# Kernel tuning notes

Measured on AMD Instinct MI355X. Metric: run time of the kernel, lower is better.

The kernel has to match this reference:

```python
import jax, jax.numpy as jnp
import numpy as np

B, N, E = 2, 50000, 800000
IN, HID, OUT = 128, 64, 1
EPS = 1e-5


def setup_inputs() -> dict:
    key = jax.random.key(0)
    ks = jax.random.split(key, 13)
    x = jax.random.normal(ks[0], (B, N, IN), jnp.float32)
    edge_index = jax.random.randint(ks[1], (2, E), 0, N, dtype=jnp.int64)
    edge_weight = 0.1 * jax.random.normal(ks[2], (E,), jnp.float32)  # nn.Parameter, pre-exp
    W1 = jax.random.normal(ks[3], (IN, HID), jnp.float32) / np.sqrt(IN)
    b1 = jnp.zeros((HID,), jnp.float32)
    W2 = jax.random.normal(ks[4], (HID, HID), jnp.float32) / np.sqrt(HID)
    b2 = jnp.zeros((HID,), jnp.float32)
    g1 = jnp.ones((HID,), jnp.float32)
    be1 = jnp.zeros((HID,), jnp.float32)
    g2 = jnp.ones((HID,), jnp.float32)
    be2 = jnp.zeros((HID,), jnp.float32)
    Wc = jax.random.normal(ks[5], (HID, OUT), jnp.float32) / np.sqrt(HID)
    bc = jnp.zeros((OUT,), jnp.float32)
    return {"x": x, "edge_weight": edge_weight, "W1": W1, "b1": b1,
            "W2": W2, "b2": b2, "g1": g1, "be1": be1, "g2": g2, "be2": be2,
            "Wc": Wc, "bc": bc, "edge_index": edge_index}


def reference(x, edge_weight, W1, b1, W2, b2, g1, be1, g2, be2, Wc, bc, edge_index):
    n = x.shape[1]
    row, col = edge_index[0], edge_index[1]
    ew = jnp.exp(edge_weight)
    # GCN normalization with self-loops (fill_value=1), as in PyG gcn_norm
    loop = jnp.arange(n)
    rows = jnp.concatenate([row, loop])
    cols = jnp.concatenate([col, loop])
    w = jnp.concatenate([ew, jnp.ones((n,), ew.dtype)])
    deg = jax.ops.segment_sum(w, cols, num_segments=n)
    dinv = 1.0 / jnp.sqrt(deg)  # deg >= 1 due to self-loops
    norm = dinv[rows] * w * dinv[cols]  # [E+N]

    def conv(h, W, b):
        h = h @ W                                  # [B, N, H]
        msg = h[:, rows, :] * norm[None, :, None]  # gather + weight  [B, E+N, H]
        agg = jnp.zeros_like(h).at[:, cols, :].add(msg)  # scatter-add
        return agg + b

    def bn(h, g, be):  # BatchNorm1d over flattened (B*N, H), training-mode stats
        h2 = h.reshape(-1, h.shape[-1])
        m = h2.mean(axis=0)
        v = h2.var(axis=0)
        return (((h2 - m) / jnp.sqrt(v + EPS)) * g + be).reshape(h.shape)

    h = jax.nn.relu(conv(x, W1, b1))
    h = bn(h, g1, be1)  # dropout is identity in eval
    h = jax.nn.relu(conv(h, W2, b2))
    h = bn(h, g2, be2)
    out = (h @ Wc + bc)[..., 0]  # squeeze(-1) -> [B, N]
    return out
```

## Files before the change

kernel.cpp:

```cpp
#include <hip/hip_runtime.h>
#include <hip/hip_fp16.h>
#include <cstdint>
#include <cstddef>


#define CAP  64
#define OCAP 65536
#define BN_EPS 1e-5f

static __device__ __forceinline__ unsigned h2u(__half2 h) {
  union { __half2 h; unsigned u; } c; c.h = h; return c.u;
}
static __device__ __forceinline__ __half2 u2h(unsigned u) {
  union { unsigned u; __half2 h; } c; c.u = u; return c.h;
}

__global__ void k_fill(const float* __restrict__ ew, const int* __restrict__ ei,
                       int* __restrict__ cnt, int2* __restrict__ pairs,
                       int* __restrict__ ofl_cnt, int* __restrict__ ofl_list, int E) {
  int i0 = blockIdx.x * 1024 + threadIdx.x;
  int r[4], c[4];
  float w[4];
  bool ok[4];
#pragma unroll
  for (int j = 0; j < 4; ++j) {
    int e = i0 + j * 256;
    ok[j] = e < E;
    if (ok[j]) {
      r[j] = ei[e];
      c[j] = ei[(size_t)E + e];
      w[j] = expf(ew[e]);
    }
  }
  int pos[4];
#pragma unroll
  for (int j = 0; j < 4; ++j)
    if (ok[j]) pos[j] = atomicAdd(&cnt[c[j]], 1);
#pragma unroll
  for (int j = 0; j < 4; ++j) {
    if (!ok[j]) continue;
    if (pos[j] < CAP) {
      pairs[(size_t)c[j] * CAP + pos[j]] = make_int2(r[j], __float_as_int(w[j]));
    } else {
      int o = atomicAdd(ofl_cnt, 1);
      if (o < OCAP) ofl_list[o] = i0 + j * 256;
    }
  }
}

__global__ void k_degb(const int2* __restrict__ pairs, const int* __restrict__ cnt,
                       float* __restrict__ deg, int N) {
  int node = blockIdx.x * 4 + (threadIdx.x >> 6);
  if (node >= N) return;
  int lane = threadIdx.x & 63;
  int n = cnt[node];
  n = n > CAP ? CAP : n;
  float v = 0.0f;
  if (lane < n) v = __int_as_float(pairs[(size_t)node * CAP + lane].y);
#pragma unroll
  for (int off = 32; off > 0; off >>= 1) v += __shfl_xor(v, off, 64);
  if (lane == 0) deg[node] = v + 1.0f;
}

__global__ void k_dego(const float* __restrict__ ew, const int* __restrict__ ei,
                       const int* __restrict__ ofl_cnt, const int* __restrict__ ofl_list,
                       float* __restrict__ deg, int E) {
  int tot = *ofl_cnt;
  if (tot > OCAP) tot = OCAP;
  for (int i = blockIdx.x * blockDim.x + threadIdx.x; i < tot;
       i += gridDim.x * blockDim.x) {
    int e = ofl_list[i];
    atomicAdd(&deg[ei[(size_t)E + e]], expf(ew[e]));
  }
}

__global__ void k_dinvf(float* __restrict__ deg, int N) {
  int i = blockIdx.x * blockDim.x + threadIdx.x;
  if (i < N) deg[i] = rsqrtf(deg[i]);
}

template<int CIN, bool TR, bool PERM>
__global__ void k_gemm(const void* __restrict__ in_, const float* __restrict__ W,
                       __half* __restrict__ out, int nrows, int N,
                       const float* __restrict__ bias, const float* __restrict__ scsh) {
  constexpr int RT = 64;
  constexpr int KC = 64;
  constexpr int NCH = CIN / KC;
  constexpr int S = KC + 4;
  __shared__ float ws[KC * 64];
  __shared__ float xs[RT * S];

  int tid = threadIdx.x;
  int row0 = blockIdx.x * RT;
  int rg = tid >> 4;
  int cg = tid & 15;
  int c0 = cg * 4;
  int r0 = rg * 4;

  float acc[4][4];
#pragma unroll
  for (int i = 0; i < 4; ++i)
#pragma unroll
    for (int j = 0; j < 4; ++j) acc[i][j] = 0.0f;

  for (int ch = 0; ch < NCH; ++ch) {
    if (ch) __syncthreads();
    const float4* Wp = (const float4*)(W + (size_t)ch * KC * 64);
    for (int s = tid; s < KC * 16; s += 256)
      ((float4*)ws)[s] = Wp[s];
    for (int s = tid; s < RT * 16; s += 256) {
      int r = s >> 4, k4 = s & 15;
      int gr = row0 + r;
      int kg = ch * KC + k4 * 4;
      float4 v = make_float4(0.f, 0.f, 0.f, 0.f);
      if (gr < nrows) {
        if (TR) {
          const __half* in = (const __half*)in_;
          uint2 u = *(const uint2*)(in + (size_t)gr * CIN + kg);
          float2 fa = __half22float2(u2h(u.x));
          float2 fb = __half22float2(u2h(u.y));
          v = make_float4(fa.x, fa.y, fb.x, fb.y);
        } else {
          const float* in = (const float*)in_;
          v = *(const float4*)(in + (size_t)gr * CIN + kg);
        }
      }
      if (TR) {
        float4 bb = *(const float4*)(bias + kg);
        float4 sc = *(const float4*)(scsh + kg);
        float4 sh = *(const float4*)(scsh + 64 + kg);
        v.x = fmaxf(v.x + bb.x, 0.f) * sc.x + sh.x;
        v.y = fmaxf(v.y + bb.y, 0.f) * sc.y + sh.y;
        v.z = fmaxf(v.z + bb.z, 0.f) * sc.z + sh.z;
        v.w = fmaxf(v.w + bb.w, 0.f) * sc.w + sh.w;
      }
      *(float4*)&xs[r * S + k4 * 4] = v;
    }
    __syncthreads();

#pragma unroll 2
    for (int kk = 0; kk < KC; kk += 4) {
      float4 wv0 = *(const float4*)&ws[(kk + 0) * 64 + c0];
      float4 wv1 = *(const float4*)&ws[(kk + 1) * 64 + c0];
      float4 wv2 = *(const float4*)&ws[(kk + 2) * 64 + c0];
      float4 wv3 = *(const float4*)&ws[(kk + 3) * 64 + c0];
#pragma unroll
      for (int i = 0; i < 4; ++i) {
        float4 xv = *(const float4*)&xs[(r0 + i) * S + kk];
        acc[i][0] = fmaf(xv.x, wv0.x, acc[i][0]);
        acc[i][1] = fmaf(xv.x, wv0.y, acc[i][1]);
        acc[i][2] = fmaf(xv.x, wv0.z, acc[i][2]);
        acc[i][3] = fmaf(xv.x, wv0.w, acc[i][3]);
        acc[i][0] = fmaf(xv.y, wv1.x, acc[i][0]);
        acc[i][1] = fmaf(xv.y, wv1.y, acc[i][1]);
        acc[i][2] = fmaf(xv.y, wv1.z, acc[i][2]);
        acc[i][3] = fmaf(xv.y, wv1.w, acc[i][3]);
        acc[i][0] = fmaf(xv.z, wv2.x, acc[i][0]);
        acc[i][1] = fmaf(xv.z, wv2.y, acc[i][1]);
        acc[i][2] = fmaf(xv.z, wv2.z, acc[i][2]);
        acc[i][3] = fmaf(xv.z, wv2.w, acc[i][3]);
        acc[i][0] = fmaf(xv.w, wv3.x, acc[i][0]);
        acc[i][1] = fmaf(xv.w, wv3.y, acc[i][1]);
        acc[i][2] = fmaf(xv.w, wv3.z, acc[i][2]);
        acc[i][3] = fmaf(xv.w, wv3.w, acc[i][3]);
      }
    }
  }

#pragma unroll
  for (int i = 0; i < 4; ++i) {
    int gr = row0 + r0 + i;
    if (gr < nrows) {
      int orow = PERM ? ((gr < N) ? gr * 2 : (gr - N) * 2 + 1) : gr;
      __half2 h01 = __floats2half2_rn(acc[i][0], acc[i][1]);
      __half2 h23 = __floats2half2_rn(acc[i][2], acc[i][3]);
      *(uint2*)(out + (size_t)orow * 64 + c0) = make_uint2(h2u(h01), h2u(h23));
    }
  }
}

__global__ void k_agg(const __half* __restrict__ h, const int2* __restrict__ pairs,
                      const int* __restrict__ cnt, const float* __restrict__ dinv,
                      __half* __restrict__ raw, int N) {
  int node = blockIdx.x * 4 + (threadIdx.x >> 6);
  if (node >= N) return;
  int lane = threadIdx.x & 63;
  const __half2* hv = (const __half2*)h;
  float dc = dinv[node];
  float2 self = __half22float2(hv[(size_t)node * 64 + lane]);
  float2 acc = make_float2(self.x * dc, self.y * dc);
  int n = cnt[node];
  n = n > CAP ? CAP : n;
  const int2* pp = pairs + (size_t)node * CAP;
  int k = 0;
  for (; k + 8 <= n; k += 8) {
    int2 p[8];
#pragma unroll
    for (int q = 0; q < 8; ++q) p[q] = pp[k + q];
    float dr[8];
#pragma unroll
    for (int q = 0; q < 8; ++q) dr[q] = dinv[p[q].x];
    __half2 v[8];
#pragma unroll
    for (int q = 0; q < 8; ++q) v[q] = hv[(size_t)p[q].x * 64 + lane];
#pragma unroll
    for (int q = 0; q < 8; ++q) {
      float w = __int_as_float(p[q].y) * dr[q];
      float2 f = __half22float2(v[q]);
      acc.x = fmaf(w, f.x, acc.x);
      acc.y = fmaf(w, f.y, acc.y);
    }
  }
  for (; k < n; ++k) {
    int2 p = pp[k];
    float w = __int_as_float(p.y) * dinv[p.x];
    float2 f = __half22float2(hv[(size_t)p.x * 64 + lane]);
    acc.x = fmaf(w, f.x, acc.x);
    acc.y = fmaf(w, f.y, acc.y);
  }
  ((__half2*)raw)[(size_t)node * 64 + lane] =
      __floats2half2_rn(acc.x * dc, acc.y * dc);
}

__global__ void k_ofl(const float* __restrict__ ew, const int* __restrict__ ei,
                      const float* __restrict__ dinv, const int* __restrict__ ofl_cnt,
                      const int* __restrict__ ofl_list,
                      const __half* __restrict__ h, __half* __restrict__ raw,
                      int N, int E) {
  int tot = *ofl_cnt;
  if (tot > OCAP) tot = OCAP;
  for (int i = blockIdx.x * blockDim.x + threadIdx.x; i < tot;
       i += gridDim.x * blockDim.x) {
    int e = ofl_list[i];
    int r = ei[e];
    int c = ei[(size_t)E + e];
    float nrm = dinv[r] * expf(ew[e]) * dinv[c];
    const __half2* hr = (const __half2*)(h + (size_t)r * 128);
    unsigned* dst = (unsigned*)(raw + (size_t)c * 128);
    for (int j = 0; j < 64; ++j) {
      float2 hv2 = __half22float2(hr[j]);
      unsigned old = dst[j], assumed;
      do {
        assumed = old;
        float2 cur = __half22float2(u2h(assumed));
        __half2 nv = __floats2half2_rn(cur.x + nrm * hv2.x, cur.y + nrm * hv2.y);
        old = atomicCAS(&dst[j], assumed, h2u(nv));
      } while (old != assumed);
    }
  }
}

__global__ void k_stats(const __half* __restrict__ raw, const float* __restrict__ bias,
                        float* __restrict__ stats, int rows) {
  __shared__ float S[256], Q[256];
  int tid = threadIdx.x;
  int c = tid & 63, rg = tid >> 6;
  float s = 0.0f, q = 0.0f;
  for (int r = blockIdx.x * 4 + rg; r < rows; r += gridDim.x * 4) {
    float y = fmaxf(__half2float(raw[(size_t)r * 64 + c]) + bias[c], 0.0f);
    s += y;
    q += y * y;
  }
  S[tid] = s; Q[tid] = q;
  __syncthreads();
  if (tid < 64) {
    float ts = S[tid] + S[tid + 64] + S[tid + 128] + S[tid + 192];
    float tq = Q[tid] + Q[tid + 64] + Q[tid + 128] + Q[tid + 192];
    atomicAdd(&stats[tid], ts);
    atomicAdd(&stats[64 + tid], tq);
  }
}

__global__ void k_scale(const float* __restrict__ stats, const float* __restrict__ g,
                        const float* __restrict__ be, float* __restrict__ scsh,
                        float invCnt) {
  int c = threadIdx.x;
  if (c >= 64) return;
  float m = stats[c] * invCnt;
  float v = stats[64 + c] * invCnt - m * m;
  v = v < 0.0f ? 0.0f : v;
  float inv = rsqrtf(v + BN_EPS);
  float sc = g[c] * inv;
  scsh[c] = sc;
  scsh[64 + c] = be[c] - m * sc;
}

__global__ void k_out(const __half* __restrict__ raw, const float* __restrict__ bias,
                      const float* __restrict__ scsh, const float* __restrict__ Wc,
                      const float* __restrict__ bc, float* __restrict__ out,
                      int rows, int N) {
  int row = blockIdx.x * 4 + (threadIdx.x >> 6);
  int c = threadIdx.x & 63;
  if (row >= rows) return;
  float v = fmaxf(__half2float(raw[(size_t)row * 64 + c]) + bias[c], 0.0f)
              * scsh[c] + scsh[64 + c];
  float p = v * Wc[c];
#pragma unroll
  for (int off = 32; off > 0; off >>= 1) p += __shfl_xor(p, off, 64);
  if (c == 0) {
    int node = row >> 1, b = row & 1;
    out[(size_t)b * N + node] = p + bc[0];
  }
}

extern "C" void kernel_launch(void* const* d_in, const int* in_sizes, int n_in,
                              void* d_out, int out_size, void* d_ws, size_t ws_size,
                              hipStream_t stream) {
  const float* x   = (const float*)d_in[0];
  const float* ew  = (const float*)d_in[1];
  const float* W1  = (const float*)d_in[2];
  const float* b1  = (const float*)d_in[3];
  const float* W2  = (const float*)d_in[4];
  const float* b2  = (const float*)d_in[5];
  const float* g1  = (const float*)d_in[6];
  const float* be1 = (const float*)d_in[7];
  const float* g2  = (const float*)d_in[8];
  const float* be2 = (const float*)d_in[9];
  const float* Wc  = (const float*)d_in[10];
  const float* bc  = (const float*)d_in[11];
  const int*   ei  = (const int*)d_in[12];

  const int E  = in_sizes[1];
  const int BN = in_sizes[0] / 128;
  const int N  = BN / 2;

  char* w = (char*)d_ws;
  size_t off = 0;
  float* dinv   = (float*)(w + off); off += (size_t)N * 4;
  int*   cnt    = (int*)  (w + off); off += (size_t)N * 4;
  float* stats1 = (float*)(w + off); off += 512;
  float* stats2 = (float*)(w + off); off += 512;
  int*   oflc   = (int*)  (w + off); off += 16;
  size_t zbytes = off;
  float* scsh1  = (float*)(w + off); off += 512;
  float* scsh2  = (float*)(w + off); off += 512;
  int*   ofll   = (int*)  (w + off); off += (size_t)OCAP * 4;
  off = (off + 255) & ~(size_t)255;
  int2*   pairs = (int2*)  (w + off); off += (size_t)N * CAP * 8;
  __half* bufA  = (__half*)(w + off); off += (size_t)BN * 64 * 2;
  __half* bufB  = (__half*)(w + off); off += (size_t)BN * 64 * 2;

  float* out = (float*)d_out;

  hipMemsetAsync(w, 0, zbytes, stream);

  dim3 blk(256);
  int gE4 = (E + 1023) / 1024;
  int gN  = (N + 255) / 256;
  int gG  = (BN + 63) / 64;
  int gR  = (BN + 3) / 4;
  int gA  = (N + 3) / 4;

  k_fill<<<gE4, blk, 0, stream>>>(ew, ei, cnt, pairs, oflc, ofll, E);
  k_degb<<<gA, blk, 0, stream>>>(pairs, cnt, dinv, N);
  k_dego<<<16, blk, 0, stream>>>(ew, ei, oflc, ofll, dinv, E);
  k_dinvf<<<gN, blk, 0, stream>>>(dinv, N);

  k_gemm<128, false, true><<<gG, blk, 0, stream>>>(x, W1, bufA, BN, N, nullptr, nullptr);
  k_agg<<<gA, blk, 0, stream>>>(bufA, pairs, cnt, dinv, bufB, N);
  k_ofl<<<16, blk, 0, stream>>>(ew, ei, dinv, oflc, ofll, bufA, bufB, N, E);
  k_stats<<<400, blk, 0, stream>>>(bufB, b1, stats1, BN);
  k_scale<<<1, 64, 0, stream>>>(stats1, g1, be1, scsh1, 1.0f / (float)BN);

  k_gemm<64, true, false><<<gG, blk, 0, stream>>>(bufB, W2, bufA, BN, N, b1, scsh1);
  k_agg<<<gA, blk, 0, stream>>>(bufA, pairs, cnt, dinv, bufB, N);
  k_ofl<<<16, blk, 0, stream>>>(ew, ei, dinv, oflc, ofll, bufA, bufB, N, E);
  k_stats<<<400, blk, 0, stream>>>(bufB, b2, stats2, BN);
  k_scale<<<1, 64, 0, stream>>>(stats2, g2, be2, scsh2, 1.0f / (float)BN);

  k_out<<<gR, blk, 0, stream>>>(bufB, b2, scsh2, Wc, bc, out, BN, N);
}
```

Baseline: 362.4 us.

## Fuse first GEMM with edge fill, pack edge pairs to 32 bits, fold BN scale

Combines the first-layer GEMM and the edge bucketing fill into one launch, with blocks interleaved by role so the compute-bound and atomic-bound work can overlap. Edge pairs are packed into a single 32-bit word: a 16-bit source index and an fp16 weight. This halves the pair storage and gather traffic in the degree and aggregation kernels, but assumes node ids fit in 16 bits and rounds weights to half precision. The BN scale/shift computation moves into the last block of the stats kernel via a completion counter, removing two launches. The aggregation unroll is also widened to 12 with a 4-wide tail.

After: 366.5 us. Within noise of the previous version (+1.1%).

```diff
diff --git a/kernel.cpp b/kernel.cpp
--- a/kernel.cpp
+++ b/kernel.cpp
@@ -14,41 +14,113 @@
 static __device__ __forceinline__ __half2 u2h(unsigned u) {
   union { unsigned u; __half2 h; } c; c.u = u; return c.h;
 }
-
-__global__ void k_fill(const float* __restrict__ ew, const int* __restrict__ ei,
-                       int* __restrict__ cnt, int2* __restrict__ pairs,
-                       int* __restrict__ ofl_cnt, int* __restrict__ ofl_list, int E) {
-  int i0 = blockIdx.x * 1024 + threadIdx.x;
-  int r[4], c[4];
-  float w[4];
-  bool ok[4];
-#pragma unroll
-  for (int j = 0; j < 4; ++j) {
-    int e = i0 + j * 256;
-    ok[j] = e < E;
-    if (ok[j]) {
-      r[j] = ei[e];
-      c[j] = ei[(size_t)E + e];
-      w[j] = expf(ew[e]);
-    }
-  }
-  int pos[4];
-#pragma unroll
-  for (int j = 0; j < 4; ++j)
-    if (ok[j]) pos[j] = atomicAdd(&cnt[c[j]], 1);
-#pragma unroll
-  for (int j = 0; j < 4; ++j) {
-    if (!ok[j]) continue;
-    if (pos[j] < CAP) {
-      pairs[(size_t)c[j] * CAP + pos[j]] = make_int2(r[j], __float_as_int(w[j]));
+static __device__ __forceinline__ unsigned pack_pair(int src, float w) {
+  __half hw = __float2half_rn(w);
+  union { __half h; unsigned short s; } c; c.h = hw;
+  return ((unsigned)src << 16) | c.s;
+}
+static __device__ __forceinline__ float pair_w(unsigned p) {
+  union { unsigned short s; __half h; } c; c.s = (unsigned short)(p & 0xFFFFu);
+  return __half2float(c.h);
+}
+
+__global__ void k_mega(const float* __restrict__ x, const float* __restrict__ W,
+                       __half* __restrict__ out, int nrows, int N,
+                       const float* __restrict__ ew, const int* __restrict__ ei,
+                       int* __restrict__ cnt, unsigned* __restrict__ pairs,
+                       int* __restrict__ ofl_cnt, int* __restrict__ ofl_list,
+                       int E, int gemmBlocks, int fillBlocks) {
+  constexpr int RT = 64, KC = 64, S = KC + 4;
+  __shared__ float ws[KC * 64];
+  __shared__ float xs[RT * S];
+
+  int bid = blockIdx.x;
+  int tid = threadIdx.x;
+  int role = bid % 3;
+
+  if (role == 0) {
+    int gid = bid / 3;
+    if (gid >= gemmBlocks) return;
+    int row0 = gid * RT;
+    int rg = tid >> 4, cg = tid & 15;
+    int c0 = cg * 4, r0 = rg * 4;
+    float acc[4][4];
+#pragma unroll
+    for (int i = 0; i < 4; ++i)
+#pragma unroll
+      for (int j = 0; j < 4; ++j) acc[i][j] = 0.0f;
+
+    for (int ch = 0; ch < 2; ++ch) {
+      if (ch) __syncthreads();
+      const float4* Wp = (const float4*)(W + (size_t)ch * KC * 64);
+      for (int s = tid; s < KC * 16; s += 256)
+        ((float4*)ws)[s] = Wp[s];
+      for (int s = tid; s < RT * 16; s += 256) {
+        int r = s >> 4, k4 = s & 15;
+        int gr = row0 + r;
+        float4 v = make_float4(0.f, 0.f, 0.f, 0.f);
+        if (gr < nrows)
+          v = *(const float4*)(x + (size_t)gr * 128 + ch * KC + k4 * 4);
+        *(float4*)&xs[r * S + k4 * 4] = v;
+      }
+      __syncthreads();
+#pragma unroll 2
+      for (int kk = 0; kk < KC; kk += 4) {
+        float4 wv0 = *(const float4*)&ws[(kk + 0) * 64 + c0];
+        float4 wv1 = *(const float4*)&ws[(kk + 1) * 64 + c0];
+        float4 wv2 = *(const float4*)&ws[(kk + 2) * 64 + c0];
+        float4 wv3 = *(const float4*)&ws[(kk + 3) * 64 + c0];
+#pragma unroll
+        for (int i = 0; i < 4; ++i) {
+          float4 xv = *(const float4*)&xs[(r0 + i) * S + kk];
+          acc[i][0] = fmaf(xv.x, wv0.x, acc[i][0]);
+          acc[i][1] = fmaf(xv.x, wv0.y, acc[i][1]);
+          acc[i][2] = fmaf(xv.x, wv0.z, acc[i][2]);
+          acc[i][3] = fmaf(xv.x, wv0.w, acc[i][3]);
+          acc[i][0] = fmaf(xv.y, wv1.x, acc[i][0]);
+          acc[i][1] = fmaf(xv.y, wv1.y, acc[i][1]);
+          acc[i][2] = fmaf(xv.y, wv1.z, acc[i][2]);
+          acc[i][3] = fmaf(xv.y, wv1.w, acc[i][3]);
+          acc[i][0] = fmaf(xv.z, wv2.x, acc[i][0]);
+          acc[i][1] = fmaf(xv.z, wv2.y, acc[i][1]);
+          acc[i][2] = fmaf(xv.z, wv2.z, acc[i][2]);
+          acc[i][3] = fmaf(xv.z, wv2.w, acc[i][3]);
+          acc[i][0] = fmaf(xv.w, wv3.x, acc[i][0]);
+          acc[i][1] = fmaf(xv.w, wv3.y, acc[i][1]);
+          acc[i][2] = fmaf(xv.w, wv3.z, acc[i][2]);
+          acc[i][3] = fmaf(xv.w, wv3.w, acc[i][3]);
+        }
+      }
+    }
+#pragma unroll
+    for (int i = 0; i < 4; ++i) {
+      int gr = row0 + r0 + i;
+      if (gr < nrows) {
+        int orow = (gr < N) ? gr * 2 : (gr - N) * 2 + 1;
+        __half2 h01 = __floats2half2_rn(acc[i][0], acc[i][1]);
+        __half2 h23 = __floats2half2_rn(acc[i][2], acc[i][3]);
+        *(uint2*)(out + (size_t)orow * 64 + c0) = make_uint2(h2u(h01), h2u(h23));
+      }
+    }
+  } else {
+    int fid = (bid / 3) * 2 + role - 1;
+    if (fid >= fillBlocks) return;
+    int e = fid * 256 + tid;
+    if (e >= E) return;
+    int r = ei[e];
+    int c = ei[(size_t)E + e];
+    float w = expf(ew[e]);
+    int pos = atomicAdd(&cnt[c], 1);
+    if (pos < CAP) {
+      pairs[(size_t)c * CAP + pos] = pack_pair(r, w);
     } else {
       int o = atomicAdd(ofl_cnt, 1);
-      if (o < OCAP) ofl_list[o] = i0 + j * 256;
-    }
-  }
-}
-
-__global__ void k_degb(const int2* __restrict__ pairs, const int* __restrict__ cnt,
+      if (o < OCAP) ofl_list[o] = e;
+    }
+  }
+}
+
+__global__ void k_degb(const unsigned* __restrict__ pairs, const int* __restrict__ cnt,
                        float* __restrict__ deg, int N) {
   int node = blockIdx.x * 4 + (threadIdx.x >> 6);
   if (node >= N) return;
@@ -56,7 +128,7 @@
   int n = cnt[node];
   n = n > CAP ? CAP : n;
   float v = 0.0f;
-  if (lane < n) v = __int_as_float(pairs[(size_t)node * CAP + lane].y);
+  if (lane < n) v = pair_w(pairs[(size_t)node * CAP + lane]);
 #pragma unroll
   for (int off = 32; off > 0; off >>= 1) v += __shfl_xor(v, off, 64);
   if (lane == 0) deg[node] = v + 1.0f;
@@ -79,107 +151,85 @@
   if (i < N) deg[i] = rsqrtf(deg[i]);
 }
 
-template<int CIN, bool TR, bool PERM>
-__global__ void k_gemm(const void* __restrict__ in_, const float* __restrict__ W,
-                       __half* __restrict__ out, int nrows, int N,
-                       const float* __restrict__ bias, const float* __restrict__ scsh) {
-  constexpr int RT = 64;
-  constexpr int KC = 64;
-  constexpr int NCH = CIN / KC;
-  constexpr int S = KC + 4;
+__global__ void k_gemm2(const __half* __restrict__ in, const float* __restrict__ W,
+                        __half* __restrict__ out, int nrows,
+                        const float* __restrict__ bias, const float* __restrict__ scsh) {
+  constexpr int RT = 64, KC = 64, S = KC + 4;
   __shared__ float ws[KC * 64];
   __shared__ float xs[RT * S];
 
   int tid = threadIdx.x;
   int row0 = blockIdx.x * RT;
-  int rg = tid >> 4;
-  int cg = tid & 15;
-  int c0 = cg * 4;
-  int r0 = rg * 4;
-
+  for (int s = tid; s < KC * 16; s += 256)
+    ((float4*)ws)[s] = ((const float4*)W)[s];
+  for (int s = tid; s < RT * 16; s += 256) {
+    int r = s >> 4, k4 = s & 15;
+    int gr = row0 + r;
+    int kg = k4 * 4;
+    float4 v = make_float4(0.f, 0.f, 0.f, 0.f);
+    if (gr < nrows) {
+      uint2 u = *(const uint2*)(in + (size_t)gr * 64 + kg);
+      float2 fa = __half22float2(u2h(u.x));
+      float2 fb = __half22float2(u2h(u.y));
+      v = make_float4(fa.x, fa.y, fb.x, fb.y);
+    }
+    float4 bb = *(const float4*)(bias + kg);
+    float4 sc = *(const float4*)(scsh + kg);
+    float4 sh = *(const float4*)(scsh + 64 + kg);
+    v.x = fmaxf(v.x + bb.x, 0.f) * sc.x + sh.x;
+    v.y = fmaxf(v.y + bb.y, 0.f) * sc.y + sh.y;
+    v.z = fmaxf(v.z + bb.z, 0.f) * sc.z + sh.z;
+    v.w = fmaxf(v.w + bb.w, 0.f) * sc.w + sh.w;
+    *(float4*)&xs[r * S + kg] = v;
+  }
+  __syncthreads();
+
+  int rg = tid >> 4, cg = tid & 15;
+  int c0 = cg * 4, r0 = rg * 4;
   float acc[4][4];
 #pragma unroll
   for (int i = 0; i < 4; ++i)
 #pragma unroll
     for (int j = 0; j < 4; ++j) acc[i][j] = 0.0f;
-
-  for (int ch = 0; ch < NCH; ++ch) {
-    if (ch) __syncthreads();
-    const float4* Wp = (const float4*)(W + (size_t)ch * KC * 64);
-    for (int s = tid; s < KC * 16; s += 256)
-      ((float4*)ws)[s] = Wp[s];
-    for (int s = tid; s < RT * 16; s += 256) {
-      int r = s >> 4, k4 = s & 15;
-      int gr = row0 + r;
-      int kg = ch * KC + k4 * 4;
-      float4 v = make_float4(0.f, 0.f, 0.f, 0.f);
-      if (gr < nrows) {
-        if (TR) {
-          const __half* in = (const __half*)in_;
-          uint2 u = *(const uint2*)(in + (size_t)gr * CIN + kg);
-          float2 fa = __half22float2(u2h(u.x));
-          float2 fb = __half22float2(u2h(u.y));
-          v = make_float4(fa.x, fa.y, fb.x, fb.y);
-        } else {
-          const float* in = (const float*)in_;
-          v = *(const float4*)(in + (size_t)gr * CIN + kg);
-        }
-      }
-      if (TR) {
-        float4 bb = *(const float4*)(bias + kg);
-        float4 sc = *(const float4*)(scsh + kg);
-        float4 sh = *(const float4*)(scsh + 64 + kg);
-        v.x = fmaxf(v.x + bb.x, 0.f) * sc.x + sh.x;
-        v.y = fmaxf(v.y + bb.y, 0.f) * sc.y + sh.y;
-        v.z = fmaxf(v.z + bb.z, 0.f) * sc.z + sh.z;
-        v.w = fmaxf(v.w + bb.w, 0.f) * sc.w + sh.w;
-      }
-      *(float4*)&xs[r * S + k4 * 4] = v;
-    }
-    __syncthreads();
-
 #pragma unroll 2
-    for (int kk = 0; kk < KC; kk += 4) {
-      float4 wv0 = *(const float4*)&ws[(kk + 0) * 64 + c0];
-      float4 wv1 = *(const float4*)&ws[(kk + 1) * 64 + c0];
-      float4 wv2 = *(const float4*)&ws[(kk + 2) * 64 + c0];
-      float4 wv3 = *(const float4*)&ws[(kk + 3) * 64 + c0];
-#pragma unroll
-      for (int i = 0; i < 4; ++i) {
-        float4 xv = *(const float4*)&xs[(r0 + i) * S + kk];
-        acc[i][0] = fmaf(xv.x, wv0.x, acc[i][0]);
-        acc[i][1] = fmaf(xv.x, wv0.y, acc[i][1]);
-        acc[i][2] = fmaf(xv.x, wv0.z, acc[i][2]);
-        acc[i][3] = fmaf(xv.x, wv0.w, acc[i][3]);
-        acc[i][0] = fmaf(xv.y, wv1.x, acc[i][0]);
-        acc[i][1] = fmaf(xv.y, wv1.y, acc[i][1]);
-        acc[i][2] = fmaf(xv.y, wv1.z, acc[i][2]);
-        acc[i][3] = fmaf(xv.y, wv1.w, acc[i][3]);
-        acc[i][0] = fmaf(xv.z, wv2.x, acc[i][0]);
-        acc[i][1] = fmaf(xv.z, wv2.y, acc[i][1]);
-        acc[i][2] = fmaf(xv.z, wv2.z, acc[i][2]);
-        acc[i][3] = fmaf(xv.z, wv2.w, acc[i][3]);
-        acc[i][0] = fmaf(xv.w, wv3.x, acc[i][0]);
-        acc[i][1] = fmaf(xv.w, wv3.y, acc[i][1]);
-        acc[i][2] = fmaf(xv.w, wv3.z, acc[i][2]);
-        acc[i][3] = fmaf(xv.w, wv3.w, acc[i][3]);
-      }
-    }
-  }
-
+  for (int kk = 0; kk < KC; kk += 4) {
+    float4 wv0 = *(const float4*)&ws[(kk + 0) * 64 + c0];
+    float4 wv1 = *(const float4*)&ws[(kk + 1) * 64 + c0];
+    float4 wv2 = *(const float4*)&ws[(kk + 2) * 64 + c0];
+    float4 wv3 = *(const float4*)&ws[(kk + 3) * 64 + c0];
+#pragma unroll
+    for (int i = 0; i < 4; ++i) {
+      float4 xv = *(const float4*)&xs[(r0 + i) * S + kk];
+      acc[i][0] = fmaf(xv.x, wv0.x, acc[i][0]);
+      acc[i][1] = fmaf(xv.x, wv0.y, acc[i][1]);
+      acc[i][2] = fmaf(xv.x, wv0.z, acc[i][2]);
+      acc[i][3] = fmaf(xv.x, wv0.w, acc[i][3]);
+      acc[i][0] = fmaf(xv.y, wv1.x, acc[i][0]);
+      acc[i][1] = fmaf(xv.y, wv1.y, acc[i][1]);
+      acc[i][2] = fmaf(xv.y, wv1.z, acc[i][2]);
+      acc[i][3] = fmaf(xv.y, wv1.w, acc[i][3]);
+      acc[i][0] = fmaf(xv.z, wv2.x, acc[i][0]);
+      acc[i][1] = fmaf(xv.z, wv2.y, acc[i][1]);
+      acc[i][2] = fmaf(xv.z, wv2.z, acc[i][2]);
+      acc[i][3] = fmaf(xv.z, wv2.w, acc[i][3]);
+      acc[i][0] = fmaf(xv.w, wv3.x, acc[i][0]);
+      acc[i][1] = fmaf(xv.w, wv3.y, acc[i][1]);
+      acc[i][2] = fmaf(xv.w, wv3.z, acc[i][2]);
+      acc[i][3] = fmaf(xv.w, wv3.w, acc[i][3]);
+    }
+  }
 #pragma unroll
   for (int i = 0; i < 4; ++i) {
     int gr = row0 + r0 + i;
     if (gr < nrows) {
-      int orow = PERM ? ((gr < N) ? gr * 2 : (gr - N) * 2 + 1) : gr;
       __half2 h01 = __floats2half2_rn(acc[i][0], acc[i][1]);
       __half2 h23 = __floats2half2_rn(acc[i][2], acc[i][3]);
-      *(uint2*)(out + (size_t)orow * 64 + c0) = make_uint2(h2u(h01), h2u(h23));
-    }
-  }
-}
-
-__global__ void k_agg(const __half* __restrict__ h, const int2* __restrict__ pairs,
+      *(uint2*)(out + (size_t)gr * 64 + c0) = make_uint2(h2u(h01), h2u(h23));
+    }
+  }
+}
+
+__global__ void k_agg(const __half* __restrict__ h, const unsigned* __restrict__ pairs,
                       const int* __restrict__ cnt, const float* __restrict__ dinv,
                       __half* __restrict__ raw, int N) {
   int node = blockIdx.x * 4 + (threadIdx.x >> 6);
@@ -191,30 +241,48 @@
   float2 acc = make_float2(self.x * dc, self.y * dc);
   int n = cnt[node];
   n = n > CAP ? CAP : n;
-  const int2* pp = pairs + (size_t)node * CAP;
+  const unsigned* pp = pairs + (size_t)node * CAP;
   int k = 0;
-  for (; k + 8 <= n; k += 8) {
-    int2 p[8];
-#pragma unroll
-    for (int q = 0; q < 8; ++q) p[q] = pp[k + q];
-    float dr[8];
-#pragma unroll
-    for (int q = 0; q < 8; ++q) dr[q] = dinv[p[q].x];
-    __half2 v[8];
-#pragma unroll
-    for (int q = 0; q < 8; ++q) v[q] = hv[(size_t)p[q].x * 64 + lane];
-#pragma unroll
-    for (int q = 0; q < 8; ++q) {
-      float w = __int_as_float(p[q].y) * dr[q];
+  for (; k + 12 <= n; k += 12) {
+    unsigned p[12];
+#pragma unroll
+    for (int q = 0; q < 12; ++q) p[q] = pp[k + q];
+    float dr[12];
+#pragma unroll
+    for (int q = 0; q < 12; ++q) dr[q] = dinv[p[q] >> 16];
+    __half2 v[12];
+#pragma unroll
+    for (int q = 0; q < 12; ++q) v[q] = hv[(size_t)(p[q] >> 16) * 64 + lane];
+#pragma unroll
+    for (int q = 0; q < 12; ++q) {
+      float w = pair_w(p[q]) * dr[q];
       float2 f = __half22float2(v[q]);
       acc.x = fmaf(w, f.x, acc.x);
       acc.y = fmaf(w, f.y, acc.y);
     }
   }
+  for (; k + 4 <= n; k += 4) {
+    unsigned p[4];
+#pragma unroll
+    for (int q = 0; q < 4; ++q) p[q] = pp[k + q];
+    float dr[4];
+#pragma unroll
+    for (int q = 0; q < 4; ++q) dr[q] = dinv[p[q] >> 16];
+    __half2 v[4];
+#pragma unroll
+    for (int q = 0; q < 4; ++q) v[q] = hv[(size_t)(p[q] >> 16) * 64 + lane];
+#pragma unroll
+    for (int q = 0; q < 4; ++q) {
+      float w = pair_w(p[q]) * dr[q];
+      float2 f = __half22float2(v[q]);
+      acc.x = fmaf(w, f.x, acc.x);
+      acc.y = fmaf(w, f.y, acc.y);
+    }
+  }
   for (; k < n; ++k) {
-    int2 p = pp[k];
-    float w = __int_as_float(p.y) * dinv[p.x];
-    float2 f = __half22float2(hv[(size_t)p.x * 64 + lane]);
+    unsigned p = pp[k];
+    float w = pair_w(p) * dinv[p >> 16];
+    float2 f = __half22float2(hv[(size_t)(p >> 16) * 64 + lane]);
     acc.x = fmaf(w, f.x, acc.x);
     acc.y = fmaf(w, f.y, acc.y);
   }
@@ -251,8 +319,11 @@
 }
 
 __global__ void k_stats(const __half* __restrict__ raw, const float* __restrict__ bias,
-                        float* __restrict__ stats, int rows) {
+                        float* __restrict__ stats, const float* __restrict__ g,
+                        const float* __restrict__ be, float* __restrict__ scsh,
+                        int* __restrict__ done, float invCnt, int rows) {
   __shared__ float S[256], Q[256];
+  __shared__ int isLast;
   int tid = threadIdx.x;
   int c = tid & 63, rg = tid >> 6;
   float s = 0.0f, q = 0.0f;
@@ -269,20 +340,23 @@
     atomicAdd(&stats[tid], ts);
     atomicAdd(&stats[64 + tid], tq);
   }
-}
-
-__global__ void k_scale(const float* __restrict__ stats, const float* __restrict__ g,
-                        const float* __restrict__ be, float* __restrict__ scsh,
-                        float invCnt) {
-  int c = threadIdx.x;
-  if (c >= 64) return;
-  float m = stats[c] * invCnt;
-  float v = stats[64 + c] * invCnt - m * m;
-  v = v < 0.0f ? 0.0f : v;
-  float inv = rsqrtf(v + BN_EPS);
-  float sc = g[c] * inv;
-  scsh[c] = sc;
-  scsh[64 + c] = be[c] - m * sc;
+  __threadfence();
+  if (tid == 0) {
+    int old = atomicAdd(done, 1);
+    isLast = (old == (int)gridDim.x - 1);
+  }
+  __syncthreads();
+  if (isLast && tid < 64) {
+    __threadfence();
+    float m = atomicAdd(&stats[tid], 0.0f) * invCnt;
+    float qq = atomicAdd(&stats[64 + tid], 0.0f) * invCnt;
+    float v = qq - m * m;
+    v = v < 0.0f ? 0.0f : v;
+    float inv = rsqrtf(v + BN_EPS);
+    float sc = g[tid] * inv;
+    scsh[tid] = sc;
+    scsh[64 + tid] = be[tid] - m * sc;
+  }
 }
 
 __global__ void k_out(const __half* __restrict__ raw, const float* __restrict__ bias,
@@ -326,17 +400,19 @@
 
   char* w = (char*)d_ws;
   size_t off = 0;
-  float* dinv   = (float*)(w + off); off += (size_t)N * 4;
   int*   cnt    = (int*)  (w + off); off += (size_t)N * 4;
   float* stats1 = (float*)(w + off); off += 512;
   float* stats2 = (float*)(w + off); off += 512;
   int*   oflc   = (int*)  (w + off); off += 16;
+  int*   done1  = (int*)  (w + off); off += 16;
+  int*   done2  = (int*)  (w + off); off += 16;
   size_t zbytes = off;
+  float* dinv   = (float*)(w + off); off += (size_t)N * 4;
   float* scsh1  = (float*)(w + off); off += 512;
   float* scsh2  = (float*)(w + off); off += 512;
   int*   ofll   = (int*)  (w + off); off += (size_t)OCAP * 4;
   off = (off + 255) & ~(size_t)255;
-  int2*   pairs = (int2*)  (w + off); off += (size_t)N * CAP * 8;
+  unsigned* pairs = (unsigned*)(w + off); off += (size_t)N * CAP * 4;
   __half* bufA  = (__half*)(w + off); off += (size_t)BN * 64 * 2;
   __half* bufB  = (__half*)(w + off); off += (size_t)BN * 64 * 2;
 
@@ -345,28 +421,30 @@
   hipMemsetAsync(w, 0, zbytes, stream);
 
   dim3 blk(256);
-  int gE4 = (E + 1023) / 1024;
+  int gB = (BN + 63) / 64;
+  int fB = (E + 255) / 256;
+  int base3 = gB > (fB + 1) / 2 ? gB : (fB + 1) / 2;
+  int gMega = 3 * base3;
   int gN  = (N + 255) / 256;
-  int gG  = (BN + 63) / 64;
   int gR  = (BN + 3) / 4;
   int gA  = (N + 3) / 4;
 
-  k_fill<<<gE4, blk, 0, stream>>>(ew, ei, cnt, pairs, oflc, ofll, E);
+  k_mega<<<gMega, blk, 0, stream>>>(x, W1, bufA, BN, N, ew, ei, cnt, pairs,
+                                    oflc, ofll, E, gB, fB);
   k_degb<<<gA, blk, 0, stream>>>(pairs, cnt, dinv, N);
   k_dego<<<16, blk, 0, stream>>>(ew, ei, oflc, ofll, dinv, E);
   k_dinvf<<<gN, blk, 0, stream>>>(dinv, N);
 
-  k_gemm<128, false, true><<<gG, blk, 0, stream>>>(x, W1, bufA, BN, N, nullptr, nullptr);
   k_agg<<<gA, blk, 0, stream>>>(bufA, pairs, cnt, dinv, bufB, N);
   k_ofl<<<16, blk, 0, stream>>>(ew, ei, dinv, oflc, ofll, bufA, bufB, N, E);
-  k_stats<<<400, blk, 0, stream>>>(bufB, b1, stats1, BN);
-  k_scale<<<1, 64, 0, stream>>>(stats1, g1, be1, scsh1, 1.0f / (float)BN);
-
-  k_gemm<64, true, false><<<gG, blk, 0, stream>>>(bufB, W2, bufA, BN, N, b1, scsh1);
+  k_stats<<<400, blk, 0, stream>>>(bufB, b1, stats1, g1, be1, scsh1, done1,
+                                   1.0f / (float)BN, BN);
+
+  k_gemm2<<<gB, blk, 0, stream>>>(bufB, W2, bufA, BN, b1, scsh1);
   k_agg<<<gA, blk, 0, stream>>>(bufA, pairs, cnt, dinv, bufB, N);
   k_ofl<<<16, blk, 0, stream>>>(ew, ei, dinv, oflc, ofll, bufA, bufB, N, E);
-  k_stats<<<400, blk, 0, stream>>>(bufB, b2, stats2, BN);
-  k_scale<<<1, 64, 0, stream>>>(stats2, g2, be2, scsh2, 1.0f / (float)BN);
+  k_stats<<<400, blk, 0, stream>>>(bufB, b2, stats2, g2, be2, scsh2, done2,
+                                   1.0f / (float)BN, BN);
 
   k_out<<<gR, blk, 0, stream>>>(bufB, b2, scsh2, Wc, bc, out, BN, N);
 }
```
